# Kernel tuning notes

Measured on AMD Instinct MI355X. Metric: run time of the kernel, lower is better.

## Reference

```python
import jax, jax.numpy as jnp
import numpy as np

N_NODES = 50000
N_EDGES = 800000
N_GRAPHS = 128
IN_F = 768
NHID = 64
HID2 = NHID * 2  # 128
N_CLS = 2


def setup_inputs() -> dict:
    key = jax.random.key(0)
    ks = jax.random.split(key, 16)
    s = lambda k, shp, fan: jax.random.normal(k, shp, jnp.float32) / np.sqrt(fan)
    return {
        "x": jax.random.normal(ks[0], (N_NODES, IN_F), jnp.float32),
        "edge_index": jax.random.randint(ks[1], (2, N_EDGES), 0, N_NODES, jnp.int64),
        "batch": jnp.sort(jax.random.randint(ks[2], (N_NODES,), 0, N_GRAPHS, jnp.int64)),
        "W1": s(ks[3], (IN_F, HID2), IN_F),
        "as1": s(ks[4], (HID2,), HID2),
        "ad1": s(ks[5], (HID2,), HID2),
        "b1": jnp.zeros((HID2,), jnp.float32),
        "W2": s(ks[6], (HID2, HID2), HID2),
        "as2": s(ks[7], (HID2,), HID2),
        "ad2": s(ks[8], (HID2,), HID2),
        "b2": jnp.zeros((HID2,), jnp.float32),
        "fc1_w": s(ks[9], (HID2, NHID), HID2),
        "fc1_b": jnp.zeros((NHID,), jnp.float32),
        "fc2_w": s(ks[10], (NHID, N_CLS), NHID),
        "fc2_b": jnp.zeros((N_CLS,), jnp.float32),
    }


def _gat_conv(x, W, a_src, a_dst, b, src, dst):
    # PyG GATConv, heads=1, self-loops already included in (src, dst).
    xw = x @ W                                   # [N, F_out]
    e_src = xw @ a_src                           # [N]
    e_dst = xw @ a_dst                           # [N]
    e = jax.nn.leaky_relu(e_src[src] + e_dst[dst], 0.2)   # [E]
    m = jax.ops.segment_max(e, dst, num_segments=N_NODES)  # per-dst max (stable softmax)
    num = jnp.exp(e - m[dst])
    den = jax.ops.segment_sum(num, dst, num_segments=N_NODES)
    alpha = num / den[dst]                       # [E]
    out = jax.ops.segment_sum(alpha[:, None] * xw[src], dst, num_segments=N_NODES)
    return out + b


def reference(x, edge_index, batch, W1, as1, ad1, b1, W2, as2, ad2, b2,
              fc1_w, fc1_b, fc2_w, fc2_b):
    # add self loops (PyG GATConv default add_self_loops=True)
    loops = jnp.arange(N_NODES, dtype=edge_index.dtype)
    src = jnp.concatenate([edge_index[0], loops])
    dst = jnp.concatenate([edge_index[1], loops])

    h = jax.nn.selu(_gat_conv(x, W1, as1, ad1, b1, src, dst))
    h = jax.nn.selu(_gat_conv(h, W2, as2, ad2, b2, src, dst))

    # global mean pool over graphs
    sums = jax.ops.segment_sum(h, batch, num_segments=N_GRAPHS)          # [G, HID2]
    cnts = jax.ops.segment_sum(jnp.ones((N_NODES,), h.dtype), batch, num_segments=N_GRAPHS)
    pooled = jax.nn.selu(sums / jnp.maximum(cnts, 1.0)[:, None])

    g = jax.nn.selu(pooled @ fc1_w + fc1_b)      # dropout is identity in eval mode
    logits = g @ fc2_w + fc2_b
    return jax.nn.log_softmax(logits, axis=-1)
```

## Files before the change

kernel.cpp:

```cpp
#include <hip/hip_runtime.h>
#include <math.h>

#define N_NODES  50000
#define N_EDGES  800000
#define E_TOT    (N_EDGES + N_NODES)
#define N_GRAPHS 128
#define IN_F     768
#define HID2     128
#define NHID     64

typedef __attribute__((ext_vector_type(8))) short bf16x8;
typedef __attribute__((ext_vector_type(4))) float f32x4;
typedef __attribute__((ext_vector_type(4))) unsigned short us4;

__device__ __forceinline__ float selu_f(float x) {
    const float alpha = 1.6732632423543772f;
    const float scale = 1.0507009873554805f;
    return scale * (x > 0.f ? x : alpha * (expf(x) - 1.f));
}

__device__ __forceinline__ unsigned short f2bf(float f) {
    unsigned u = __float_as_uint(f);
    u += 0x7FFFu + ((u >> 16) & 1u);
    return (unsigned short)(u >> 16);
}
__device__ __forceinline__ float bflo(unsigned q) { return __uint_as_float(q << 16); }
__device__ __forceinline__ float bfhi(unsigned q) { return __uint_as_float(q & 0xffff0000u); }

__global__ void setup_k(const float* __restrict__ W1, const float* __restrict__ W2,
                        unsigned short* __restrict__ Wt1, unsigned short* __restrict__ Wt2,
                        unsigned* __restrict__ deg) {
    int i = blockIdx.x * blockDim.x + threadIdx.x;
    if (i < N_NODES) deg[i] = 0u;
    if (i < 128 * IN_F) {
        int n = i / IN_F, k = i - n * IN_F;
        Wt1[i] = f2bf(W1[(long)k * 128 + n]);
    }
    if (i < 128 * HID2) {
        int n = i >> 7, k = i & 127;
        Wt2[i] = f2bf(W2[(long)k * 128 + n]);
    }
}

#define LDA2 72
template<bool ABF16, bool OUTBF16>
__global__ __launch_bounds__(256) void gemm_mfma(
        const void* __restrict__ Av, const unsigned short* __restrict__ Bt,
        void* __restrict__ Cv, int M, int K,
        const float* __restrict__ a_s, const float* __restrict__ a_d,
        float* __restrict__ es, float* __restrict__ ed) {
    __shared__ unsigned short As[64 * LDA2];
    __shared__ unsigned short Bs[128 * LDA2];
    __shared__ float es_s[2][64];
    __shared__ float ed_s[2][64];
    const float* Af = (const float*)Av;
    const unsigned short* Ab = (const unsigned short*)Av;
    const int tid  = threadIdx.x;
    const int row0 = blockIdx.x * 64;
    const int w    = tid >> 6;
    const int lane = tid & 63;
    const int quad = lane >> 4;
    const int l16  = lane & 15;
    const int m_off = (w & 1) * 32;
    const int n_off = (w >> 1) * 64;
    const int nh    = w >> 1;

    f32x4 acc[2][4];
#pragma unroll
    for (int mi = 0; mi < 2; mi++)
#pragma unroll
        for (int ni = 0; ni < 4; ni++)
            acc[mi][ni] = (f32x4){0.f, 0.f, 0.f, 0.f};

    float4 aR[4];
    bf16x8 aRb[2];
    bf16x8 bR[4];
    if (ABF16) {
#pragma unroll
        for (int i = 0; i < 2; i++) {
            int p = tid + i * 256;
            int r = p >> 3, c8 = p & 7;
            int gr = row0 + r;
            aRb[i] = (gr < M) ? *(const bf16x8*)&Ab[(long)gr * K + c8 * 8]
                              : (bf16x8){0,0,0,0,0,0,0,0};
        }
    } else {
#pragma unroll
        for (int i = 0; i < 4; i++) {
            int p = tid + i * 256;
            int r = p >> 4, c4 = p & 15;
            int gr = row0 + r;
            aR[i] = (gr < M) ? *(const float4*)&Af[(long)gr * K + c4 * 4]
                             : make_float4(0.f, 0.f, 0.f, 0.f);
        }
    }
#pragma unroll
    for (int i = 0; i < 4; i++) {
        int c = tid + i * 256;
        int n = c >> 3, koff = (c & 7) * 8;
        bR[i] = *(const bf16x8*)&Bt[(long)n * K + koff];
    }

    for (int k0 = 0; k0 < K; k0 += 64) {
        if (ABF16) {
#pragma unroll
            for (int i = 0; i < 2; i++) {
                int p = tid + i * 256;
                int r = p >> 3, c8 = p & 7;
                *(bf16x8*)&As[r * LDA2 + c8 * 8] = aRb[i];
            }
        } else {
#pragma unroll
            for (int i = 0; i < 4; i++) {
                int p = tid + i * 256;
                int r = p >> 4, c4 = p & 15;
                us4 o;
                o.x = f2bf(aR[i].x); o.y = f2bf(aR[i].y);
                o.z = f2bf(aR[i].z); o.w = f2bf(aR[i].w);
                *(us4*)&As[r * LDA2 + c4 * 4] = o;
            }
        }
#pragma unroll
        for (int i = 0; i < 4; i++) {
            int c = tid + i * 256;
            int n = c >> 3, koff = (c & 7) * 8;
            *(bf16x8*)&Bs[n * LDA2 + koff] = bR[i];
        }
        __syncthreads();

        if (k0 + 64 < K) {
            int k1 = k0 + 64;
            if (ABF16) {
#pragma unroll
                for (int i = 0; i < 2; i++) {
                    int p = tid + i * 256;
                    int r = p >> 3, c8 = p & 7;
                    int gr = row0 + r;
                    aRb[i] = (gr < M) ? *(const bf16x8*)&Ab[(long)gr * K + k1 + c8 * 8]
                                      : (bf16x8){0,0,0,0,0,0,0,0};
                }
            } else {
#pragma unroll
                for (int i = 0; i < 4; i++) {
                    int p = tid + i * 256;
                    int r = p >> 4, c4 = p & 15;
                    int gr = row0 + r;
                    aR[i] = (gr < M) ? *(const float4*)&Af[(long)gr * K + k1 + c4 * 4]
                                     : make_float4(0.f, 0.f, 0.f, 0.f);
                }
            }
#pragma unroll
            for (int i = 0; i < 4; i++) {
                int c = tid + i * 256;
                int n = c >> 3, koff = (c & 7) * 8;
                bR[i] = *(const bf16x8*)&Bt[(long)n * K + k1 + koff];
            }
        }

        bf16x8 af[2][2], bfr[2][4];
#pragma unroll
        for (int kk = 0; kk < 2; kk++) {
#pragma unroll
            for (int mi = 0; mi < 2; mi++)
                af[kk][mi] = *(const bf16x8*)&As[(m_off + mi * 16 + l16) * LDA2 + kk * 32 + quad * 8];
#pragma unroll
            for (int ni = 0; ni < 4; ni++)
                bfr[kk][ni] = *(const bf16x8*)&Bs[(n_off + ni * 16 + l16) * LDA2 + kk * 32 + quad * 8];
        }
#pragma unroll
        for (int kk = 0; kk < 2; kk++)
#pragma unroll
            for (int mi = 0; mi < 2; mi++)
#pragma unroll
                for (int ni = 0; ni < 4; ni++)
                    acc[mi][ni] = __builtin_amdgcn_mfma_f32_16x16x32_bf16(
                        af[kk][mi], bfr[kk][ni], acc[mi][ni], 0, 0, 0);
        __syncthreads();
    }

    float as_v[4], ad_v[4];
#pragma unroll
    for (int ni = 0; ni < 4; ni++) {
        int col = n_off + ni * 16 + l16;
        as_v[ni] = a_s[col];
        ad_v[ni] = a_d[col];
    }

#pragma unroll
    for (int mi = 0; mi < 2; mi++)
#pragma unroll
        for (int r = 0; r < 4; r++) {
            int rl  = m_off + mi * 16 + quad * 4 + r;
            int row = row0 + rl;
            float ps = 0.f, pd = 0.f;
#pragma unroll
            for (int ni = 0; ni < 4; ni++) {
                float v = acc[mi][ni][r];
                ps = fmaf(v, as_v[ni], ps);
                pd = fmaf(v, ad_v[ni], pd);
            }
#pragma unroll
            for (int o = 1; o < 16; o <<= 1) {
                ps += __shfl_xor(ps, o);
                pd += __shfl_xor(pd, o);
            }
            if (l16 == 0) {
                es_s[nh][rl] = ps;
                ed_s[nh][rl] = pd;
            }
            if (row < M) {
                if (OUTBF16) {
                    unsigned short* C16 = (unsigned short*)Cv;
#pragma unroll
                    for (int ni = 0; ni < 4; ni++)
                        C16[(long)row * 128 + n_off + ni * 16 + l16] = f2bf(acc[mi][ni][r]);
                } else {
                    float* Cf = (float*)Cv;
#pragma unroll
                    for (int ni = 0; ni < 4; ni++)
                        Cf[(long)row * 128 + n_off + ni * 16 + l16] = acc[mi][ni][r];
                }
            }
        }
    __syncthreads();
    if (tid < 64) {
        int row = row0 + tid;
        if (row < M) {
            es[row] = es_s[0][tid] + es_s[1][tid];
            ed[row] = ed_s[0][tid] + ed_s[1][tid];
        }
    }
}

__global__ void deg_hist(const int* __restrict__ ei, unsigned* __restrict__ deg) {
    int e = blockIdx.x * blockDim.x + threadIdx.x;
    if (e < N_EDGES) atomicAdd(&deg[ei[N_EDGES + e]], 1u);
}

__global__ __launch_bounds__(256) void scan_seed(const unsigned* __restrict__ deg,
                                                 unsigned* __restrict__ row_ptr,
                                                 unsigned* __restrict__ cursor,
                                                 unsigned* __restrict__ csr_src) {
    __shared__ unsigned psum_s[4];
    __shared__ unsigned wsum[4];
    int tid = threadIdx.x;
    int wid = tid >> 6, lane = tid & 63;
    int chunk0 = blockIdx.x * 256;

    unsigned psum = 0;
    for (int i = tid; i < chunk0; i += 256) psum += deg[i] + 1u;
    for (int o = 32; o; o >>= 1) psum += __shfl_xor(psum, o);
    if (lane == 0) psum_s[wid] = psum;

    int i = chunk0 + tid;
    unsigned v = (i < N_NODES) ? deg[i] + 1u : 0u;
    unsigned x = v;
    for (int o = 1; o < 64; o <<= 1) {
        unsigned y = __shfl_up(x, o);
        if (lane >= o) x += y;
    }
    if (lane == 63) wsum[wid] = x;
    __syncthreads();
    unsigned base = psum_s[0] + psum_s[1] + psum_s[2] + psum_s[3];
    unsigned wbase = 0;
    for (int k = 0; k < wid; k++) wbase += wsum[k];
    if (i < N_NODES) {
        unsigned rp = base + wbase + x - v;
        row_ptr[i] = rp;
        csr_src[rp] = (unsigned)i;
        cursor[i] = rp + 1;
        if (i == N_NODES - 1) row_ptr[N_NODES] = rp + v;
    }
}

__global__ void csr_scatter(const int* __restrict__ ei,
                            unsigned* __restrict__ cursor, unsigned* __restrict__ csr_src) {
    int e = blockIdx.x * blockDim.x + threadIdx.x;
    if (e >= N_EDGES) return;
    int d = ei[N_EDGES + e];
    unsigned p = atomicAdd(&cursor[d], 1u);
    csr_src[p] = (unsigned)ei[e];
}

template<bool OUTBF16>
__global__ __launch_bounds__(256) void gat_agg(
        const unsigned* __restrict__ row_ptr, const unsigned* __restrict__ csr_src,
        const float* __restrict__ e_src, const float* __restrict__ e_dst,
        const unsigned short* __restrict__ xw, const float* __restrict__ bias,
        void* __restrict__ outv) {
    __shared__ float2 buf[8][32];
    int hw = threadIdx.x >> 5;
    int node = blockIdx.x * 8 + hw;
    if (node >= N_NODES) return;
    int fl = threadIdx.x & 31;
    unsigned beg = row_ptr[node];
    int deg = (int)(row_ptr[node + 1] - beg);
    float ed = e_dst[node];
    const unsigned short* xwf = xw + fl * 4;

    float ax = 0.f, ay = 0.f, az = 0.f, aw = 0.f, den = 0.f;
    for (int base = 0; base < deg; base += 32) {
        int i = base + fl;
        float num = 0.f;
        unsigned s = 0u;
        if (i < deg) {
            s = csr_src[beg + i];
            float e = e_src[s] + ed;
            e = e > 0.f ? e : 0.2f * e;
            num = __expf(e);
            den += num;
        }
        float2 pk; pk.x = num; pk.y = __uint_as_float(s);
        buf[hw][fl] = pk;

        int cnt = deg - base; if (cnt > 32) cnt = 32;
        int t = 0;
        for (; t + 8 <= cnt; t += 8) {
            float2 p0 = buf[hw][t + 0];
            float2 p1 = buf[hw][t + 1];
            float2 p2 = buf[hw][t + 2];
            float2 p3 = buf[hw][t + 3];
            float2 p4 = buf[hw][t + 4];
            float2 p5 = buf[hw][t + 5];
            float2 p6 = buf[hw][t + 6];
            float2 p7 = buf[hw][t + 7];
            uint2 q0 = *(const uint2*)&xwf[(long)__float_as_uint(p0.y) * HID2];
            uint2 q1 = *(const uint2*)&xwf[(long)__float_as_uint(p1.y) * HID2];
            uint2 q2 = *(const uint2*)&xwf[(long)__float_as_uint(p2.y) * HID2];
            uint2 q3 = *(const uint2*)&xwf[(long)__float_as_uint(p3.y) * HID2];
            uint2 q4 = *(const uint2*)&xwf[(long)__float_as_uint(p4.y) * HID2];
            uint2 q5 = *(const uint2*)&xwf[(long)__float_as_uint(p5.y) * HID2];
            uint2 q6 = *(const uint2*)&xwf[(long)__float_as_uint(p6.y) * HID2];
            uint2 q7 = *(const uint2*)&xwf[(long)__float_as_uint(p7.y) * HID2];
            ax = fmaf(p0.x, bflo(q0.x), ax); ay = fmaf(p0.x, bfhi(q0.x), ay);
            az = fmaf(p0.x, bflo(q0.y), az); aw = fmaf(p0.x, bfhi(q0.y), aw);
            ax = fmaf(p1.x, bflo(q1.x), ax); ay = fmaf(p1.x, bfhi(q1.x), ay);
            az = fmaf(p1.x, bflo(q1.y), az); aw = fmaf(p1.x, bfhi(q1.y), aw);
            ax = fmaf(p2.x, bflo(q2.x), ax); ay = fmaf(p2.x, bfhi(q2.x), ay);
            az = fmaf(p2.x, bflo(q2.y), az); aw = fmaf(p2.x, bfhi(q2.y), aw);
            ax = fmaf(p3.x, bflo(q3.x), ax); ay = fmaf(p3.x, bfhi(q3.x), ay);
            az = fmaf(p3.x, bflo(q3.y), az); aw = fmaf(p3.x, bfhi(q3.y), aw);
            ax = fmaf(p4.x, bflo(q4.x), ax); ay = fmaf(p4.x, bfhi(q4.x), ay);
            az = fmaf(p4.x, bflo(q4.y), az); aw = fmaf(p4.x, bfhi(q4.y), aw);
            ax = fmaf(p5.x, bflo(q5.x), ax); ay = fmaf(p5.x, bfhi(q5.x), ay);
            az = fmaf(p5.x, bflo(q5.y), az); aw = fmaf(p5.x, bfhi(q5.y), aw);
            ax = fmaf(p6.x, bflo(q6.x), ax); ay = fmaf(p6.x, bfhi(q6.x), ay);
            az = fmaf(p6.x, bflo(q6.y), az); aw = fmaf(p6.x, bfhi(q6.y), aw);
            ax = fmaf(p7.x, bflo(q7.x), ax); ay = fmaf(p7.x, bfhi(q7.x), ay);
            az = fmaf(p7.x, bflo(q7.y), az); aw = fmaf(p7.x, bfhi(q7.y), aw);
        }
        for (; t < cnt; t++) {
            float2 p = buf[hw][t];
            uint2 q = *(const uint2*)&xwf[(long)__float_as_uint(p.y) * HID2];
            ax = fmaf(p.x, bflo(q.x), ax); ay = fmaf(p.x, bfhi(q.x), ay);
            az = fmaf(p.x, bflo(q.y), az); aw = fmaf(p.x, bfhi(q.y), aw);
        }
    }
    for (int o = 16; o; o >>= 1) den += __shfl_xor(den, o);
    float inv = 1.f / den;
    float v0 = selu_f(fmaf(ax, inv, bias[fl * 4 + 0]));
    float v1 = selu_f(fmaf(ay, inv, bias[fl * 4 + 1]));
    float v2 = selu_f(fmaf(az, inv, bias[fl * 4 + 2]));
    float v3 = selu_f(fmaf(aw, inv, bias[fl * 4 + 3]));
    if (OUTBF16) {
        uint2 o;
        o.x = ((unsigned)f2bf(v1) << 16) | (unsigned)f2bf(v0);
        o.y = ((unsigned)f2bf(v3) << 16) | (unsigned)f2bf(v2);
        *(uint2*)((unsigned short*)outv + (long)node * HID2 + fl * 4) = o;
    } else {
        float4 o = make_float4(v0, v1, v2, v3);
        *(float4*)((float*)outv + (long)node * HID2 + fl * 4) = o;
    }
}

__global__ __launch_bounds__(256) void pool_head(
        const float* __restrict__ h, const int* __restrict__ batch,
        const float* __restrict__ fc1w, const float* __restrict__ fc1b,
        const float* __restrict__ fc2w, const float* __restrict__ fc2b,
        float* __restrict__ out) {
    __shared__ float pooled_s[HID2];
    __shared__ float part[HID2];
    __shared__ float g_s[NHID];
    int g = blockIdx.x;
    int lo = 0, hi = N_NODES;
    while (lo < hi) { int mid = (lo + hi) >> 1; if (batch[mid] < g) lo = mid + 1; else hi = mid; }
    int start = lo;
    hi = N_NODES;
    while (lo < hi) { int mid = (lo + hi) >> 1; if (batch[mid] < g + 1) lo = mid + 1; else hi = mid; }
    int end = lo;

    int f = threadIdx.x & 127, half = threadIdx.x >> 7;
    float acc = 0.f;
    for (int n = start + half; n < end; n += 2) acc += h[(long)n * HID2 + f];
    if (half == 0) part[f] = acc;
    __syncthreads();
    if (half == 1) {
        float c = (float)(end - start);
        c = c > 1.f ? c : 1.f;
        pooled_s[f] = selu_f((part[f] + acc) / c);
    }
    __syncthreads();
    int j = threadIdx.x;
    if (j < NHID) {
        float a = fc1b[j];
#pragma unroll
        for (int k = 0; k < HID2; k++) a = fmaf(pooled_s[k], fc1w[k * NHID + j], a);
        g_s[j] = selu_f(a);
    }
    __syncthreads();
    if (j == 0) {
        float l0 = fc2b[0], l1 = fc2b[1];
#pragma unroll
        for (int k = 0; k < NHID; k++) {
            float v = g_s[k];
            l0 = fmaf(v, fc2w[2 * k + 0], l0);
            l1 = fmaf(v, fc2w[2 * k + 1], l1);
        }
        float m = fmaxf(l0, l1);
        float lse = m + logf(expf(l0 - m) + expf(l1 - m));
        out[g * 2 + 0] = l0 - lse;
        out[g * 2 + 1] = l1 - lse;
    }
}

extern "C" void kernel_launch(void* const* d_in, const int* in_sizes, int n_in,
                              void* d_out, int out_size, void* d_ws, size_t ws_size,
                              hipStream_t stream) {
    const float* x     = (const float*)d_in[0];
    const int*   ei    = (const int*)d_in[1];
    const int*   batch = (const int*)d_in[2];
    const float* W1    = (const float*)d_in[3];
    const float* as1   = (const float*)d_in[4];
    const float* ad1   = (const float*)d_in[5];
    const float* b1    = (const float*)d_in[6];
    const float* W2    = (const float*)d_in[7];
    const float* as2   = (const float*)d_in[8];
    const float* ad2   = (const float*)d_in[9];
    const float* b2    = (const float*)d_in[10];
    const float* fc1w  = (const float*)d_in[11];
    const float* fc1b  = (const float*)d_in[12];
    const float* fc2w  = (const float*)d_in[13];
    const float* fc2b  = (const float*)d_in[14];
    float* out = (float*)d_out;

    const long NH = (long)N_NODES * HID2;
    unsigned short* xwb = (unsigned short*)d_ws;
    unsigned short* h1b = xwb + NH;
    float*    B2      = (float*)(h1b + NH);
    float*    es1     = B2 + NH;
    float*    ed1     = es1 + N_NODES;
    float*    es2     = ed1 + N_NODES;
    float*    ed2     = es2 + N_NODES;
    unsigned* deg     = (unsigned*)(ed2 + N_NODES);
    unsigned* cursor  = deg + N_NODES;
    unsigned* row_ptr = cursor + N_NODES;
    unsigned* csr_src = row_ptr + N_NODES + 1;
    unsigned short* Wt1 = (unsigned short*)(csr_src + E_TOT);
    unsigned short* Wt2 = Wt1 + 128 * IN_F;

    const int TB = 256;
    const int gNode = (N_NODES + TB - 1) / TB;
    const int gEdge = (N_EDGES + TB - 1) / TB;
    const int gGemm = (N_NODES + 63) / 64;
    const int gAgg  = (N_NODES + 7) / 8;

    setup_k<<<(128 * IN_F + TB - 1) / TB, TB, 0, stream>>>(W1, W2, Wt1, Wt2, deg);
    deg_hist<<<gEdge, TB, 0, stream>>>(ei, deg);
    scan_seed<<<gNode, TB, 0, stream>>>(deg, row_ptr, cursor, csr_src);
    csr_scatter<<<gEdge, TB, 0, stream>>>(ei, cursor, csr_src);

    gemm_mfma<false, true><<<gGemm, 256, 0, stream>>>(x, Wt1, xwb, N_NODES, IN_F,
                                                      as1, ad1, es1, ed1);
    gat_agg<true><<<gAgg, TB, 0, stream>>>(row_ptr, csr_src, es1, ed1, xwb, b1, h1b);

    gemm_mfma<true, true><<<gGemm, 256, 0, stream>>>(h1b, Wt2, xwb, N_NODES, HID2,
                                                     as2, ad2, es2, ed2);
    gat_agg<false><<<gAgg, TB, 0, stream>>>(row_ptr, csr_src, es2, ed2, xwb, b2, B2);

    pool_head<<<N_GRAPHS, 256, 0, stream>>>(B2, batch, fc1w, fc1b, fc2w, fc2b, out);
}
```

Baseline: 526.3 us.

## Double GEMM row tile to 128, convert A early, vectorize pooling

The MFMA GEMM tile grows from 64 to 128 rows per block, with each wave now computing 4x4 MFMA tiles. This reuses the B (weight) tile across twice as many rows and halves the number of blocks. The fp32 A prefetch is converted to bf16 at load time, which shrinks the prefetch registers but raises register pressure and lowers occupancy. The pooling kernel now reads h with float4 loads over 8 row groups and reduces them in shared memory.

```diff
diff --git a/kernel.cpp b/kernel.cpp
--- a/kernel.cpp
+++ b/kernel.cpp
@@ -49,35 +49,35 @@
         void* __restrict__ Cv, int M, int K,
         const float* __restrict__ a_s, const float* __restrict__ a_d,
         float* __restrict__ es, float* __restrict__ ed) {
-    __shared__ unsigned short As[64 * LDA2];
+    __shared__ unsigned short As[128 * LDA2];
     __shared__ unsigned short Bs[128 * LDA2];
-    __shared__ float es_s[2][64];
-    __shared__ float ed_s[2][64];
+    __shared__ float es_s[2][128];
+    __shared__ float ed_s[2][128];
     const float* Af = (const float*)Av;
     const unsigned short* Ab = (const unsigned short*)Av;
     const int tid  = threadIdx.x;
-    const int row0 = blockIdx.x * 64;
+    const int row0 = blockIdx.x * 128;
     const int w    = tid >> 6;
     const int lane = tid & 63;
     const int quad = lane >> 4;
     const int l16  = lane & 15;
-    const int m_off = (w & 1) * 32;
+    const int m_off = (w & 1) * 64;
     const int n_off = (w >> 1) * 64;
     const int nh    = w >> 1;
 
-    f32x4 acc[2][4];
-#pragma unroll
-    for (int mi = 0; mi < 2; mi++)
+    f32x4 acc[4][4];
+#pragma unroll
+    for (int mi = 0; mi < 4; mi++)
 #pragma unroll
         for (int ni = 0; ni < 4; ni++)
             acc[mi][ni] = (f32x4){0.f, 0.f, 0.f, 0.f};
 
-    float4 aR[4];
-    bf16x8 aRb[2];
+    us4 aRc[8];
+    bf16x8 aRb[4];
     bf16x8 bR[4];
     if (ABF16) {
 #pragma unroll
-        for (int i = 0; i < 2; i++) {
+        for (int i = 0; i < 4; i++) {
             int p = tid + i * 256;
             int r = p >> 3, c8 = p & 7;
             int gr = row0 + r;
@@ -86,12 +86,14 @@
         }
     } else {
 #pragma unroll
-        for (int i = 0; i < 4; i++) {
+        for (int i = 0; i < 8; i++) {
             int p = tid + i * 256;
             int r = p >> 4, c4 = p & 15;
             int gr = row0 + r;
-            aR[i] = (gr < M) ? *(const float4*)&Af[(long)gr * K + c4 * 4]
-                             : make_float4(0.f, 0.f, 0.f, 0.f);
+            float4 v = (gr < M) ? *(const float4*)&Af[(long)gr * K + c4 * 4]
+                                : make_float4(0.f, 0.f, 0.f, 0.f);
+            us4 o; o.x = f2bf(v.x); o.y = f2bf(v.y); o.z = f2bf(v.z); o.w = f2bf(v.w);
+            aRc[i] = o;
         }
     }
 #pragma unroll
@@ -104,20 +106,17 @@
     for (int k0 = 0; k0 < K; k0 += 64) {
         if (ABF16) {
 #pragma unroll
-            for (int i = 0; i < 2; i++) {
+            for (int i = 0; i < 4; i++) {
                 int p = tid + i * 256;
                 int r = p >> 3, c8 = p & 7;
                 *(bf16x8*)&As[r * LDA2 + c8 * 8] = aRb[i];
             }
         } else {
 #pragma unroll
-            for (int i = 0; i < 4; i++) {
+            for (int i = 0; i < 8; i++) {
                 int p = tid + i * 256;
                 int r = p >> 4, c4 = p & 15;
-                us4 o;
-                o.x = f2bf(aR[i].x); o.y = f2bf(aR[i].y);
-                o.z = f2bf(aR[i].z); o.w = f2bf(aR[i].w);
-                *(us4*)&As[r * LDA2 + c4 * 4] = o;
+                *(us4*)&As[r * LDA2 + c4 * 4] = aRc[i];
             }
         }
 #pragma unroll
@@ -132,7 +131,7 @@
             int k1 = k0 + 64;
             if (ABF16) {
 #pragma unroll
-                for (int i = 0; i < 2; i++) {
+                for (int i = 0; i < 4; i++) {
                     int p = tid + i * 256;
                     int r = p >> 3, c8 = p & 7;
                     int gr = row0 + r;
@@ -141,12 +140,14 @@
                 }
             } else {
 #pragma unroll
-                for (int i = 0; i < 4; i++) {
+                for (int i = 0; i < 8; i++) {
                     int p = tid + i * 256;
                     int r = p >> 4, c4 = p & 15;
                     int gr = row0 + r;
-                    aR[i] = (gr < M) ? *(const float4*)&Af[(long)gr * K + k1 + c4 * 4]
-                                     : make_float4(0.f, 0.f, 0.f, 0.f);
+                    float4 v = (gr < M) ? *(const float4*)&Af[(long)gr * K + k1 + c4 * 4]
+                                        : make_float4(0.f, 0.f, 0.f, 0.f);
+                    us4 o; o.x = f2bf(v.x); o.y = f2bf(v.y); o.z = f2bf(v.z); o.w = f2bf(v.w);
+                    aRc[i] = o;
                 }
             }
 #pragma unroll
@@ -157,11 +158,11 @@
             }
         }
 
-        bf16x8 af[2][2], bfr[2][4];
+        bf16x8 af[2][4], bfr[2][4];
 #pragma unroll
         for (int kk = 0; kk < 2; kk++) {
 #pragma unroll
-            for (int mi = 0; mi < 2; mi++)
+            for (int mi = 0; mi < 4; mi++)
                 af[kk][mi] = *(const bf16x8*)&As[(m_off + mi * 16 + l16) * LDA2 + kk * 32 + quad * 8];
 #pragma unroll
             for (int ni = 0; ni < 4; ni++)
@@ -170,7 +171,7 @@
 #pragma unroll
         for (int kk = 0; kk < 2; kk++)
 #pragma unroll
-            for (int mi = 0; mi < 2; mi++)
+            for (int mi = 0; mi < 4; mi++)
 #pragma unroll
                 for (int ni = 0; ni < 4; ni++)
                     acc[mi][ni] = __builtin_amdgcn_mfma_f32_16x16x32_bf16(
@@ -187,7 +188,7 @@
     }
 
 #pragma unroll
-    for (int mi = 0; mi < 2; mi++)
+    for (int mi = 0; mi < 4; mi++)
 #pragma unroll
         for (int r = 0; r < 4; r++) {
             int rl  = m_off + mi * 16 + quad * 4 + r;
@@ -223,7 +224,7 @@
             }
         }
     __syncthreads();
-    if (tid < 64) {
+    if (tid < 128) {
         int row = row0 + tid;
         if (row < M) {
             es[row] = es_s[0][tid] + es_s[1][tid];
@@ -378,8 +379,8 @@
         const float* __restrict__ fc1w, const float* __restrict__ fc1b,
         const float* __restrict__ fc2w, const float* __restrict__ fc2b,
         float* __restrict__ out) {
+    __shared__ float part4[8][32][4];
     __shared__ float pooled_s[HID2];
-    __shared__ float part[HID2];
     __shared__ float g_s[NHID];
     int g = blockIdx.x;
     int lo = 0, hi = N_NODES;
@@ -389,15 +390,31 @@
     while (lo < hi) { int mid = (lo + hi) >> 1; if (batch[mid] < g + 1) lo = mid + 1; else hi = mid; }
     int end = lo;
 
-    int f = threadIdx.x & 127, half = threadIdx.x >> 7;
-    float acc = 0.f;
-    for (int n = start + half; n < end; n += 2) acc += h[(long)n * HID2 + f];
-    if (half == 0) part[f] = acc;
+    int l = threadIdx.x & 31, half = threadIdx.x >> 5;
+    const float4* h4 = (const float4*)h;
+    float a0 = 0.f, a1 = 0.f, a2 = 0.f, a3 = 0.f;
+    for (int n = start + half; n < end; n += 8) {
+        float4 v = h4[(long)n * 32 + l];
+        a0 += v.x; a1 += v.y; a2 += v.z; a3 += v.w;
+    }
+    part4[half][l][0] = a0; part4[half][l][1] = a1;
+    part4[half][l][2] = a2; part4[half][l][3] = a3;
     __syncthreads();
-    if (half == 1) {
+    if (threadIdx.x < 32) {
+        int q = threadIdx.x;
+        float s0 = 0.f, s1 = 0.f, s2 = 0.f, s3 = 0.f;
+#pragma unroll
+        for (int k = 0; k < 8; k++) {
+            s0 += part4[k][q][0]; s1 += part4[k][q][1];
+            s2 += part4[k][q][2]; s3 += part4[k][q][3];
+        }
         float c = (float)(end - start);
         c = c > 1.f ? c : 1.f;
-        pooled_s[f] = selu_f((part[f] + acc) / c);
+        float invc = 1.f / c;
+        pooled_s[q * 4 + 0] = selu_f(s0 * invc);
+        pooled_s[q * 4 + 1] = selu_f(s1 * invc);
+        pooled_s[q * 4 + 2] = selu_f(s2 * invc);
+        pooled_s[q * 4 + 3] = selu_f(s3 * invc);
     }
     __syncthreads();
     int j = threadIdx.x;
@@ -461,7 +478,7 @@
     const int TB = 256;
     const int gNode = (N_NODES + TB - 1) / TB;
     const int gEdge = (N_EDGES + TB - 1) / TB;
-    const int gGemm = (N_NODES + 63) / 64;
+    const int gGemm = (N_NODES + 127) / 128;
     const int gAgg  = (N_NODES + 7) / 8;
 
     setup_k<<<(128 * IN_F + TB - 1) / TB, TB, 0, stream>>>(W1, W2, Wt1, Wt2, deg);
```

Result: faster. 483.9 us (-8.1%).
